# Performance work log

Measured on AMD Instinct MI355X. Metric: run time of the kernel, lower is better.

The kernel has to match this reference:

```python
import jax, jax.numpy as jnp
import numpy as np

BS, VARNUM, EMB_DIM, SEED_DIM, N_HEADS = 32, 16384, 128, 128, 16


def setup_inputs() -> dict:
    key = jax.random.key(0)
    k1, k2, k3, k4 = jax.random.split(key, 4)
    query_seed = jax.random.normal(k1, (BS, SEED_DIM), dtype=jnp.float32)
    embeddings = jax.random.normal(k2, (BS, VARNUM, EMB_DIM), dtype=jnp.float32)
    # mask over varnum//2 base variables; 1 = keep, 0 = mask out
    attn_mask = jax.random.randint(k3, (BS, VARNUM // 2), 0, 2, dtype=jnp.int32)
    # xavier_normal_ init: std = sqrt(2 / (fan_in + fan_out))
    xavier_std = float(np.sqrt(2.0 / (EMB_DIM + SEED_DIM)))
    w_qs = jax.random.normal(k4, (N_HEADS, EMB_DIM, SEED_DIM), dtype=jnp.float32) * xavier_std
    return {"query_seed": query_seed, "embeddings": embeddings,
            "attn_mask": attn_mask, "w_qs": w_qs}


def _l2_normalize(x):
    # x / ||x||_2 along last dim (no eps, matching torch source)
    return x / jnp.linalg.norm(x, axis=-1, keepdims=True)


def reference(query_seed, embeddings, attn_mask, w_qs):
    bs, varnum, emb_dim = embeddings.shape
    n_heads = w_qs.shape[0]

    norm_embs = _l2_normalize(embeddings)                      # [bs, varnum, emb]
    # mm(w_qs.view(-1, seed), seed.T).T.view(bs, n_heads, emb) == einsum
    qs = jnp.tanh(jnp.einsum("hes,bs->bhe", w_qs, query_seed))  # [bs, heads, emb]
    norm_qs = _l2_normalize(qs)

    # orthogonality loss between head queries
    gram = jnp.einsum("bhe,bge->bhg", norm_qs, norm_qs)        # [bs, h, h]
    diff = gram - jnp.eye(n_heads, dtype=gram.dtype)
    loss = jnp.sum(diff * diff) / bs

    # cosine-similarity attention
    attn = jnp.einsum("bhe,bve->bhv", norm_qs, norm_embs)      # [bs, h, varnum]
    mask_full = jnp.concatenate([attn_mask, attn_mask], axis=1)[:, None, :]  # [bs,1,varnum]
    attn = jnp.where(mask_full == 0, -jnp.inf, attn)
    final_attn = jax.nn.softmax(attn, axis=-1)
    rc = jnp.einsum("bhv,bve->bhe", final_attn, embeddings)    # values = embeddings
    return rc, loss
```

## Files before the change

kernel.cpp:

```cpp
#include <hip/hip_runtime.h>
#include <hip/hip_bf16.h>
#include <cstdint>

#define BS     32
#define VARNUM 16384
#define EMB    128
#define SEEDD  128
#define NH     16
#define HALFV  8192

#define NCHUNK 32
#define VT     (VARNUM / NCHUNK)
#define TV     64
#define NTILE  (VT / TV)

#define EST 2080
#define PST 144

#define OFF_NORMQ 0
#define SZ_NORMQ  (BS*NH*EMB*4)
#define OFF_LOSSP (OFF_NORMQ + SZ_NORMQ)
#define SZ_LOSSP  256
#define OFF_LPART (OFF_LOSSP + SZ_LOSSP)
#define SZ_LPART  (BS*NCHUNK*NH*4)
#define OFF_PACC  (OFF_LPART + SZ_LPART)
#define SZ_PACC   ((size_t)BS*NCHUNK*NH*EMB*4)

typedef __attribute__((ext_vector_type(8))) short bf16x8;
typedef __attribute__((ext_vector_type(4))) float f32x4;

#define BAR() do { \
    asm volatile("s_waitcnt lgkmcnt(0)" ::: "memory"); \
    __builtin_amdgcn_s_barrier(); \
} while (0)

static __device__ __forceinline__ uint16_t f2bf(float f) {
    uint32_t u = __float_as_uint(f);
    return (uint16_t)((u + 0x7FFFu + ((u >> 16) & 1u)) >> 16);
}
static __device__ __forceinline__ uint32_t packbf(float a, float b) {
    __hip_bfloat162 h = __float22bfloat162_rn(make_float2(a, b));
    uint32_t u;
    __builtin_memcpy(&u, &h, 4);
    return u;
}
static __device__ __forceinline__ float dot4(float4 a, float4 b) {
    return a.x*b.x + a.y*b.y + a.z*b.z + a.w*b.w;
}

__global__ __launch_bounds__(128) void k1_q(const float* __restrict__ seed,
                                            const float* __restrict__ wqs,
                                            float* __restrict__ normq) {
    const int bh = blockIdx.x;
    const int b = bh >> 4, h = bh & 15;
    const int e = threadIdx.x;
    __shared__ __align__(16) float s_seed[SEEDD];
    s_seed[e] = seed[b*SEEDD + e];
    __syncthreads();
    const float4* w4 = (const float4*)(wqs + ((size_t)(h*EMB + e))*SEEDD);
    const float4* s4 = (const float4*)s_seed;
    float acc = 0.f;
    #pragma unroll
    for (int j = 0; j < SEEDD/4; ++j) acc += dot4(w4[j], s4[j]);
    float t = tanhf(acc);
    float sq = t*t;
    #pragma unroll
    for (int off = 32; off; off >>= 1) sq += __shfl_xor(sq, off);
    __shared__ float s_part[2];
    if ((threadIdx.x & 63) == 0) s_part[threadIdx.x >> 6] = sq;
    __syncthreads();
    float tot = s_part[0] + s_part[1];
    normq[((size_t)b*NH + h)*EMB + e] = t * rsqrtf(tot);
}

__global__ __launch_bounds__(256) void k2_loss(const float* __restrict__ normq,
                                               float* __restrict__ lossp) {
    const int b = blockIdx.x;
    const int h = threadIdx.x >> 4, g = threadIdx.x & 15;
    const float4* qh = (const float4*)(normq + ((size_t)b*NH + h)*EMB);
    const float4* qg = (const float4*)(normq + ((size_t)b*NH + g)*EMB);
    float d = 0.f;
    #pragma unroll
    for (int j = 0; j < EMB/4; ++j) d += dot4(qh[j], qg[j]);
    d -= (h == g) ? 1.f : 0.f;
    float sq = d*d;
    #pragma unroll
    for (int off = 32; off; off >>= 1) sq += __shfl_xor(sq, off);
    __shared__ float sp[4];
    if ((threadIdx.x & 63) == 0) sp[threadIdx.x >> 6] = sq;
    __syncthreads();
    if (threadIdx.x == 0) lossp[b] = sp[0] + sp[1] + sp[2] + sp[3];
}

__global__ __launch_bounds__(256, 4) void k_fused(const float* __restrict__ emb,
                                                  const int* __restrict__ mask,
                                                  const float* __restrict__ normq,
                                                  float* __restrict__ pacc,
                                                  float* __restrict__ lpart) {
    const int chunk = blockIdx.x, b = blockIdx.y;
    const int tid = threadIdx.x;
    const int w   = tid >> 6;
    const int l   = tid & 63;
    const int lhi = l >> 4;
    const int llo = l & 15;

    __shared__ __align__(16) unsigned char Elds[2][8*EST];
    __shared__ __align__(16) unsigned char Plds[16*PST];
    __shared__ __align__(16) float nsq[TV];
    __shared__ float lred[4][NH];

    bf16x8 qf[4];
    {
        const float* qrow = normq + ((size_t)b*NH + llo)*EMB;
        #pragma unroll
        for (int f = 0; f < 4; ++f) {
            const float4* qs = (const float4*)(qrow + f*32 + lhi*8);
            float4 a = qs[0], c = qs[1];
            bf16x8 t;
            t[0]=(short)f2bf(a.x); t[1]=(short)f2bf(a.y); t[2]=(short)f2bf(a.z); t[3]=(short)f2bf(a.w);
            t[4]=(short)f2bf(c.x); t[5]=(short)f2bf(c.y); t[6]=(short)f2bf(c.z); t[7]=(short)f2bf(c.w);
            qf[f] = t;
        }
    }

    f32x4 acc0 = {0.f,0.f,0.f,0.f};
    f32x4 acc1 = {0.f,0.f,0.f,0.f};
    float Lh = 0.f;

    const float* embB  = emb + (size_t)b*VARNUM*EMB;
    const int*   maskB = mask + b*HALFV;
    const int    r0    = tid >> 4;
    const int    cb    = tid & 15;

    int    mk[4];
    float4 pfa[4], pfb[4];
    {
        const int vg00 = chunk*VT;
        #pragma unroll
        for (int rep = 0; rep < 4; ++rep)
            mk[rep] = maskB[(vg00 + rep*16 + r0) & (HALFV-1)];
        #pragma unroll
        for (int rep = 0; rep < 4; ++rep) {
            const int vg = vg00 + rep*16 + r0;
            const float4* src = (const float4*)(embB + (size_t)(mk[rep] ? vg : vg00)*EMB + cb*8);
            pfa[rep] = src[0]; pfb[rep] = src[1];
        }
    }

    for (int t = 0; t < NTILE; ++t) {
        const int vg0n = chunk*VT + (t+1)*TV;
        unsigned char* Ebuf = Elds[t & 1];

        int mkn[4];
        if (t + 1 < NTILE) {
            #pragma unroll
            for (int rep = 0; rep < 4; ++rep)
                mkn[rep] = maskB[(vg0n + rep*16 + r0) & (HALFV-1)];
        }

        #pragma unroll
        for (int rep = 0; rep < 4; ++rep) {
            const int row = rep*16 + r0;
            float4 x0 = pfa[rep], x1 = pfb[rep];
            float sq = dot4(x0,x0) + dot4(x1,x1);
            sq += __shfl_xor(sq, 1); sq += __shfl_xor(sq, 2);
            sq += __shfl_xor(sq, 4); sq += __shfl_xor(sq, 8);
            if (cb == 0) nsq[row] = mk[rep] ? sq : 0.f;
            uint32_t d0 = packbf(x0.x, x0.y), d1 = packbf(x0.z, x0.w);
            uint32_t d2 = packbf(x1.x, x1.y), d3 = packbf(x1.z, x1.w);
            *(uint4*)(Ebuf + (cb>>1)*EST + row*32 + (cb&1)*16) = make_uint4(d0,d1,d2,d3);
        }

        if (t + 1 < NTILE) {
            #pragma unroll
            for (int rep = 0; rep < 4; ++rep) {
                const int vg = vg0n + rep*16 + r0;
                const float4* src = (const float4*)(embB + (size_t)(mkn[rep] ? vg : vg0n)*EMB + cb*8);
                pfa[rep] = src[0]; pfb[rep] = src[1];
                mk[rep]  = mkn[rep];
            }
        }
        BAR();

        f32x4 s = {0.f,0.f,0.f,0.f};
        #pragma unroll
        for (int f = 0; f < 4; ++f) {
            const int eblk = 2*f + (lhi >> 1);
            bf16x8 a = *(const bf16x8*)(Ebuf + eblk*EST + (w*16 + llo)*32 + (lhi&1)*16);
            s = __builtin_amdgcn_mfma_f32_16x16x32_bf16(a, qf[f], s, 0, 0, 0);
        }
        f32x4 nn = *(const f32x4*)(&nsq[w*16 + lhi*4]);
        float p[4];
        #pragma unroll
        for (int r = 0; r < 4; ++r)
            p[r] = (nn[r] > 0.f) ? __expf(s[r]*rsqrtf(nn[r]) - 1.f) : 0.f;
        uint32_t u0 = packbf(p[0], p[1]), u1 = packbf(p[2], p[3]);
        Lh += __uint_as_float(u0 << 16) + __uint_as_float(u0 & 0xFFFF0000u)
            + __uint_as_float(u1 << 16) + __uint_as_float(u1 & 0xFFFF0000u);
        {
            unsigned char* pdst = Plds + llo*PST + (w*16 + lhi*4)*2;
            *(uint32_t*)(pdst)     = u0;
            *(uint32_t*)(pdst + 4) = u1;
        }
        BAR();

        #pragma unroll
        for (int kf = 0; kf < 2; ++kf) {
            bf16x8 pa = *(const bf16x8*)(Plds + llo*PST + kf*64 + lhi*16);
            #pragma unroll
            for (int et = 0; et < 2; ++et) {
                const unsigned char* base = Ebuf + (w*2 + et)*EST + llo*2;
                bf16x8 bb;
                #pragma unroll
                for (int i = 0; i < 8; ++i)
                    bb[i] = *(const short*)(base + (size_t)(kf*32 + lhi*8 + i)*32);
                if (et == 0) acc0 = __builtin_amdgcn_mfma_f32_16x16x32_bf16(pa, bb, acc0, 0, 0, 0);
                else         acc1 = __builtin_amdgcn_mfma_f32_16x16x32_bf16(pa, bb, acc1, 0, 0, 0);
            }
        }
    }

    float* pout = pacc + (((size_t)b*NCHUNK + chunk)*NH)*EMB;
    #pragma unroll
    for (int r = 0; r < 4; ++r) {
        pout[(lhi*4 + r)*EMB + w*32 + llo]      = acc0[r];
        pout[(lhi*4 + r)*EMB + w*32 + 16 + llo] = acc1[r];
    }
    Lh += __shfl_xor(Lh, 16);
    Lh += __shfl_xor(Lh, 32);
    if (l < 16) lred[w][l] = Lh;
    BAR();
    if (tid < 16)
        lpart[((size_t)b*NCHUNK + chunk)*NH + tid] =
            lred[0][tid] + lred[1][tid] + lred[2][tid] + lred[3][tid];
}

__global__ __launch_bounds__(128) void k6_out(const float* __restrict__ pacc,
                                              const float* __restrict__ lpart,
                                              const float* __restrict__ lossp,
                                              float* __restrict__ out) {
    const int bh = blockIdx.x;
    const int b = bh >> 4, h = bh & 15;
    const int e = threadIdx.x;
    float L = 0.f;
    #pragma unroll
    for (int c = 0; c < NCHUNK; ++c) L += lpart[((size_t)b*NCHUNK + c)*NH + h];
    float acc = 0.f;
    for (int k = 0; k < NCHUNK; ++k)
        acc += pacc[(((size_t)b*NCHUNK + k)*NH + h)*EMB + e];
    out[((size_t)b*NH + h)*EMB + e] = acc / L;
    if (bh == 0 && e < 64) {
        float v = (e < BS) ? lossp[e] : 0.f;
        #pragma unroll
        for (int off = 32; off; off >>= 1) v += __shfl_xor(v, off);
        if (e == 0) out[BS*NH*EMB] = v / (float)BS;
    }
}

extern "C" void kernel_launch(void* const* d_in, const int* in_sizes, int n_in,
                              void* d_out, int out_size, void* d_ws, size_t ws_size,
                              hipStream_t stream) {
    const float* seed = (const float*)d_in[0];
    const float* emb  = (const float*)d_in[1];
    const int*   mask = (const int*)d_in[2];
    const float* wqs  = (const float*)d_in[3];
    float* out = (float*)d_out;

    char* ws = (char*)d_ws;
    float* normq = (float*)(ws + OFF_NORMQ);
    float* lossp = (float*)(ws + OFF_LOSSP);
    float* lpart = (float*)(ws + OFF_LPART);
    float* pacc  = (float*)(ws + OFF_PACC);

    k1_q<<<BS*NH, 128, 0, stream>>>(seed, wqs, normq);
    k2_loss<<<BS, 256, 0, stream>>>(normq, lossp);
    k_fused<<<dim3(NCHUNK, BS), 256, 0, stream>>>(emb, mask, normq, pacc, lpart);
    k6_out<<<BS*NH, 128, 0, stream>>>(pacc, lpart, lossp, out);
}
```

Before: 51.13 us.

## Load embedding rows in MFMA fragment layout and drop one barrier per tile

Each thread now loads the embedding row it will use as its MFMA A-operand, so the score MFMA takes fragments straight from registers instead of reading them back from LDS. Row norms are reduced across lanes with two shuffles instead of four. The P buffer is double-buffered and LDS rows are stored permuted to match the new read pattern in the second MFMA, which lets the barrier between the LDS write and the score computation go away. The trade-off is more live registers, extra LDS for the second P buffer, and a new permuted row mapping that has to stay consistent between the LDS write and the PV read.

```diff
diff --git a/kernel.cpp b/kernel.cpp
--- a/kernel.cpp
+++ b/kernel.cpp
@@ -105,9 +105,12 @@
     const int llo = l & 15;
 
     __shared__ __align__(16) unsigned char Elds[2][8*EST];
-    __shared__ __align__(16) unsigned char Plds[16*PST];
+    __shared__ __align__(16) unsigned char Plds[2][16*PST];
     __shared__ __align__(16) float nsq[TV];
     __shared__ float lred[4][NH];
+
+    const int rr = w*16 + llo;
+    const int rp = (rr & 32) | ((rr >> 3) & 3) | ((rr & 7) << 2);
 
     bf16x8 qf[4];
     {
@@ -129,66 +132,59 @@
 
     const float* embB  = emb + (size_t)b*VARNUM*EMB;
     const int*   maskB = mask + b*HALFV;
-    const int    r0    = tid >> 4;
-    const int    cb    = tid & 15;
-
-    int    mk[4];
+
+    int    mk;
     float4 pfa[4], pfb[4];
     {
-        const int vg00 = chunk*VT;
-        #pragma unroll
-        for (int rep = 0; rep < 4; ++rep)
-            mk[rep] = maskB[(vg00 + rep*16 + r0) & (HALFV-1)];
-        #pragma unroll
-        for (int rep = 0; rep < 4; ++rep) {
-            const int vg = vg00 + rep*16 + r0;
-            const float4* src = (const float4*)(embB + (size_t)(mk[rep] ? vg : vg00)*EMB + cb*8);
-            pfa[rep] = src[0]; pfb[rep] = src[1];
+        const int vg = chunk*VT + rr;
+        mk = maskB[vg & (HALFV-1)];
+        const float* rowp = embB + (size_t)(mk ? vg : (chunk*VT + w*16))*EMB;
+        #pragma unroll
+        for (int f = 0; f < 4; ++f) {
+            const float4* src = (const float4*)(rowp + f*32 + lhi*8);
+            pfa[f] = src[0]; pfb[f] = src[1];
         }
     }
 
     for (int t = 0; t < NTILE; ++t) {
-        const int vg0n = chunk*VT + (t+1)*TV;
         unsigned char* Ebuf = Elds[t & 1];
-
-        int mkn[4];
+        unsigned char* Pbuf = Plds[t & 1];
+
+        int mkn = 0;
+        if (t + 1 < NTILE)
+            mkn = maskB[(chunk*VT + (t+1)*TV + rr) & (HALFV-1)];
+
+        bf16x8 ef[4];
+        float sq = 0.f;
+        #pragma unroll
+        for (int f = 0; f < 4; ++f) {
+            float4 x0 = pfa[f], x1 = pfb[f];
+            sq += dot4(x0,x0) + dot4(x1,x1);
+            uint4 dd = make_uint4(packbf(x0.x,x0.y), packbf(x0.z,x0.w),
+                                  packbf(x1.x,x1.y), packbf(x1.z,x1.w));
+            *(uint4*)(Ebuf + (2*f + (lhi>>1))*EST + rp*32 + (lhi&1)*16) = dd;
+            __builtin_memcpy(&ef[f], &dd, 16);
+        }
+        sq += __shfl_xor(sq, 16);
+        sq += __shfl_xor(sq, 32);
+        if (l < 16) nsq[w*16 + llo] = mk ? sq : 0.f;
+
         if (t + 1 < NTILE) {
+            const int vg = chunk*VT + (t+1)*TV + rr;
+            const float* rowp = embB + (size_t)(mkn ? vg : (chunk*VT + (t+1)*TV + w*16))*EMB;
             #pragma unroll
-            for (int rep = 0; rep < 4; ++rep)
-                mkn[rep] = maskB[(vg0n + rep*16 + r0) & (HALFV-1)];
-        }
-
-        #pragma unroll
-        for (int rep = 0; rep < 4; ++rep) {
-            const int row = rep*16 + r0;
-            float4 x0 = pfa[rep], x1 = pfb[rep];
-            float sq = dot4(x0,x0) + dot4(x1,x1);
-            sq += __shfl_xor(sq, 1); sq += __shfl_xor(sq, 2);
-            sq += __shfl_xor(sq, 4); sq += __shfl_xor(sq, 8);
-            if (cb == 0) nsq[row] = mk[rep] ? sq : 0.f;
-            uint32_t d0 = packbf(x0.x, x0.y), d1 = packbf(x0.z, x0.w);
-            uint32_t d2 = packbf(x1.x, x1.y), d3 = packbf(x1.z, x1.w);
-            *(uint4*)(Ebuf + (cb>>1)*EST + row*32 + (cb&1)*16) = make_uint4(d0,d1,d2,d3);
-        }
-
-        if (t + 1 < NTILE) {
-            #pragma unroll
-            for (int rep = 0; rep < 4; ++rep) {
-                const int vg = vg0n + rep*16 + r0;
-                const float4* src = (const float4*)(embB + (size_t)(mkn[rep] ? vg : vg0n)*EMB + cb*8);
-                pfa[rep] = src[0]; pfb[rep] = src[1];
-                mk[rep]  = mkn[rep];
+            for (int f = 0; f < 4; ++f) {
+                const float4* src = (const float4*)(rowp + f*32 + lhi*8);
+                pfa[f] = src[0]; pfb[f] = src[1];
             }
-        }
-        BAR();
+            mk = mkn;
+        }
 
         f32x4 s = {0.f,0.f,0.f,0.f};
         #pragma unroll
-        for (int f = 0; f < 4; ++f) {
-            const int eblk = 2*f + (lhi >> 1);
-            bf16x8 a = *(const bf16x8*)(Ebuf + eblk*EST + (w*16 + llo)*32 + (lhi&1)*16);
-            s = __builtin_amdgcn_mfma_f32_16x16x32_bf16(a, qf[f], s, 0, 0, 0);
-        }
+        for (int f = 0; f < 4; ++f)
+            s = __builtin_amdgcn_mfma_f32_16x16x32_bf16(ef[f], qf[f], s, 0, 0, 0);
+
         f32x4 nn = *(const f32x4*)(&nsq[w*16 + lhi*4]);
         float p[4];
         #pragma unroll
@@ -198,22 +194,23 @@
         Lh += __uint_as_float(u0 << 16) + __uint_as_float(u0 & 0xFFFF0000u)
             + __uint_as_float(u1 << 16) + __uint_as_float(u1 & 0xFFFF0000u);
         {
-            unsigned char* pdst = Plds + llo*PST + (w*16 + lhi*4)*2;
+            unsigned char* pdst = Pbuf + llo*PST + (w*16 + lhi*4)*2;
             *(uint32_t*)(pdst)     = u0;
             *(uint32_t*)(pdst + 4) = u1;
         }
+
         BAR();
 
         #pragma unroll
         for (int kf = 0; kf < 2; ++kf) {
-            bf16x8 pa = *(const bf16x8*)(Plds + llo*PST + kf*64 + lhi*16);
+            bf16x8 pa = *(const bf16x8*)(Pbuf + llo*PST + kf*64 + lhi*16);
             #pragma unroll
             for (int et = 0; et < 2; ++et) {
-                const unsigned char* base = Ebuf + (w*2 + et)*EST + llo*2;
+                const unsigned char* base = Ebuf + (2*w + et)*EST + llo*2;
                 bf16x8 bb;
                 #pragma unroll
                 for (int i = 0; i < 8; ++i)
-                    bb[i] = *(const short*)(base + (size_t)(kf*32 + lhi*8 + i)*32);
+                    bb[i] = *(const short*)(base + (size_t)(kf*32 + lhi + i*4)*32);
                 if (et == 0) acc0 = __builtin_amdgcn_mfma_f32_16x16x32_bf16(pa, bb, acc0, 0, 0, 0);
                 else         acc1 = __builtin_amdgcn_mfma_f32_16x16x32_bf16(pa, bb, acc1, 0, 0, 0);
             }
```

After: 53.25 us. +4.2%, slower.
